# Kernel tuning notes

Hardware: AMD Instinct MI355X
Metric: run time of the kernel (lower is better)

The kernel has to match this reference:

```python
import jax, jax.numpy as jnp
import numpy as np

B, T, I, H = 64, 512, 1024, 2048


def setup_inputs() -> dict:
    key = jax.random.key(0)
    ks = jax.random.split(key, 6)
    s = 1.0 / np.sqrt(H).astype(np.float32)
    return {
        "input": jax.random.normal(ks[0], (B, T, I), jnp.float32),
        "internal": jax.random.normal(ks[1], (B, T), jnp.float32) * 0.1,
        "w_ih": jax.random.uniform(ks[2], (H, I), jnp.float32, -s, s),
        "w_hh": jax.random.uniform(ks[3], (H, H), jnp.float32, -s, s),
        "b_ih": jax.random.uniform(ks[4], (H,), jnp.float32, -s, s),
        "b_hh": jax.random.uniform(ks[5], (H,), jnp.float32, -s, s),
        "h0": jnp.zeros((1, B, H), jnp.float32),
        "trunc": 64,
    }


def reference(input, internal, w_ih, w_hh, b_ih, b_hh, h0, trunc):
    # input: [B, T, I]; internal: [B, T] scalar-per-step drive; h0: [1, B, H]
    Tlen = input.shape[1]
    # Hoist the input projection out of the recurrence (same math, one big GEMM).
    x_proj = jnp.einsum('bti,hi->bth', input, w_ih) + b_ih  # [B, T, H]
    # Truncated-BPTT boundaries: state is detached when i % trunc == 0.
    detach_mask = (jnp.arange(Tlen) % trunc) == 0  # [T] bool

    def step(h, xs):
        xp, noise, m = xs  # xp: [B, H], noise: [B], m: scalar bool
        # detach state at truncation boundary (no-op in forward pass)
        h = jnp.where(m, jax.lax.stop_gradient(h), h)
        h_new = jnp.tanh(xp + noise[:, None] + h @ w_hh.T + b_hh)
        return h_new, h_new

    h_last, outs = jax.lax.scan(
        step, h0[0], (x_proj.transpose(1, 0, 2), internal.T, detach_mask))
    # outputs: [B, T, H], final state: [1, B, H]
    return outs.transpose(1, 0, 2), h_last[None]
```

## Files before the change

kernel.cpp:

```cpp
#include <hip/hip_runtime.h>
#include <hip/hip_bf16.h>
#include <math.h>

#define Bb 64
#define Tt 512
#define Ii 1024
#define Hh 2048
#define NBLK 128

typedef __attribute__((ext_vector_type(8))) short bf16x8;
typedef __attribute__((ext_vector_type(8))) unsigned short ushort8;
typedef __attribute__((ext_vector_type(4))) float f32x4;

__device__ __forceinline__ unsigned short f2bf(float x) {
    unsigned int u = __float_as_uint(x);
    unsigned int r = u + 0x7fffu + ((u >> 16) & 1u);
    return (unsigned short)(r >> 16);
}

__global__ __launch_bounds__(256) void cvt_kernel(
    const float* __restrict__ src, unsigned short* __restrict__ dst)
{
    const int i = (blockIdx.x * 256 + threadIdx.x) * 4;
    float4 v = *(const float4*)(src + i);
    ushort4 o;
    o.x = f2bf(v.x); o.y = f2bf(v.y); o.z = f2bf(v.z); o.w = f2bf(v.w);
    *(ushort4*)(dst + i) = o;
}

__global__ __launch_bounds__(1024) void init_flags(unsigned int* flags) {
    flags[threadIdx.x] = 0u;
}

__global__ __launch_bounds__(256, 2) void xproj_kernel(
    const float* __restrict__ A,
    const unsigned short* __restrict__ Wbf,
    const float* __restrict__ bias,
    float* __restrict__ out)
{
    __shared__ unsigned short As[128 * 40];
    __shared__ unsigned short Bs[128 * 40];

    const int tid  = threadIdx.x;
    const int lane = tid & 63;
    const int wid  = tid >> 6;
    const int wm   = wid & 1;
    const int wn   = wid >> 1;
    const int rlo  = lane & 15;
    const int khi  = lane >> 4;

    const int m0 = blockIdx.y * 128;
    const int n0 = blockIdx.x * 128;

    f32x4 acc[4][4];
    #pragma unroll
    for (int i = 0; i < 4; ++i)
        #pragma unroll
        for (int j = 0; j < 4; ++j) acc[i][j] = (f32x4)0.f;

    for (int k0 = 0; k0 < Ii; k0 += 32) {
        #pragma unroll
        for (int p = 0; p < 4; ++p) {
            const int flat = p * 256 + tid;
            const int row  = flat >> 3;
            const int c4   = flat & 7;
            float4 v = *(const float4*)(A + (size_t)(m0 + row) * Ii + k0 + c4 * 4);
            ushort4 o;
            o.x = f2bf(v.x); o.y = f2bf(v.y); o.z = f2bf(v.z); o.w = f2bf(v.w);
            *(ushort4*)(As + row * 40 + c4 * 4) = o;
        }
        #pragma unroll
        for (int p = 0; p < 2; ++p) {
            const int flat = p * 256 + tid;
            const int row  = flat >> 2;
            const int c8   = flat & 3;
            ushort8 v = *(const ushort8*)(Wbf + (size_t)(n0 + row) * Ii + k0 + c8 * 8);
            *(ushort8*)(Bs + row * 40 + c8 * 8) = v;
        }
        __syncthreads();

        bf16x8 af[4], bfr[4];
        #pragma unroll
        for (int i = 0; i < 4; ++i)
            af[i] = *(const bf16x8*)(As + (wm * 64 + i * 16 + rlo) * 40 + khi * 8);
        #pragma unroll
        for (int j = 0; j < 4; ++j)
            bfr[j] = *(const bf16x8*)(Bs + (wn * 64 + j * 16 + rlo) * 40 + khi * 8);
        #pragma unroll
        for (int i = 0; i < 4; ++i)
            #pragma unroll
            for (int j = 0; j < 4; ++j)
                acc[i][j] = __builtin_amdgcn_mfma_f32_16x16x32_bf16(
                    af[i], bfr[j], acc[i][j], 0, 0, 0);
        __syncthreads();
    }

    #pragma unroll
    for (int j = 0; j < 4; ++j) {
        const int col = n0 + wn * 64 + j * 16 + rlo;
        const float bj = bias[col];
        #pragma unroll
        for (int i = 0; i < 4; ++i) {
            #pragma unroll
            for (int r = 0; r < 4; ++r) {
                const int m = m0 + wm * 64 + i * 16 + khi * 4 + r;
                out[(size_t)m * Hh + col] = acc[i][j][r] + bj;
            }
        }
    }
}

#define LD_FRAG(dst, base, OFF)                                               \
    asm volatile("global_load_dwordx4 %0, %1, off offset:" OFF " sc0 sc1"     \
                 : "=v"(dst) : "v"(base))

#define LD_FRAG_C(dst, base, OFF)                                             \
    asm volatile("global_load_dwordx4 %0, %1, off offset:" OFF                \
                 : "=v"(dst) : "v"(base))

#define DRAIN16(a)                                                            \
    asm volatile("s_waitcnt vmcnt(0)"                                         \
                 : "+v"(a[0][0]), "+v"(a[0][1]), "+v"(a[0][2]), "+v"(a[0][3]),\
                   "+v"(a[0][4]), "+v"(a[0][5]), "+v"(a[0][6]), "+v"(a[0][7]),\
                   "+v"(a[1][0]), "+v"(a[1][1]), "+v"(a[1][2]), "+v"(a[1][3]),\
                   "+v"(a[1][4]), "+v"(a[1][5]), "+v"(a[1][6]), "+v"(a[1][7]) \
                 :: "memory");                                                \
    __builtin_amdgcn_sched_barrier(0)

#define RAW_BARRIER()                                                         \
    asm volatile("s_waitcnt lgkmcnt(0)\n\ts_barrier" ::: "memory")

__global__ __launch_bounds__(512, 2) void rnn_persistent(
    const unsigned short* __restrict__ w_bf,
    unsigned short* __restrict__ h_bf,
    const float* __restrict__ b_hh,
    const float* __restrict__ internal,
    float* __restrict__ out,
    unsigned int* __restrict__ flags)
{
    __shared__ f32x4 red4[8 * 256];

    const int tid  = threadIdx.x;
    const int lane = tid & 63;
    const int wid  = tid >> 6;
    const int rlo  = lane & 15;
    const int khi  = lane >> 4;
    const int blk  = blockIdx.x;
    const int rh   = blk & 1;
    const int cg   = blk >> 1;

    bf16x8 wf[2][8];
    {
        const unsigned short* w0 =
            w_bf + (size_t)(cg * 32 + rlo) * Hh + wid * 256 + khi * 8;
        const unsigned short* w1 = w0 + (size_t)16 * Hh;
        LD_FRAG_C(wf[0][0], w0, "0");   LD_FRAG_C(wf[0][1], w0, "64");
        LD_FRAG_C(wf[0][2], w0, "128"); LD_FRAG_C(wf[0][3], w0, "192");
        LD_FRAG_C(wf[0][4], w0, "256"); LD_FRAG_C(wf[0][5], w0, "320");
        LD_FRAG_C(wf[0][6], w0, "384"); LD_FRAG_C(wf[0][7], w0, "448");
        LD_FRAG_C(wf[1][0], w1, "0");   LD_FRAG_C(wf[1][1], w1, "64");
        LD_FRAG_C(wf[1][2], w1, "128"); LD_FRAG_C(wf[1][3], w1, "192");
        LD_FRAG_C(wf[1][4], w1, "256"); LD_FRAG_C(wf[1][5], w1, "320");
        LD_FRAG_C(wf[1][6], w1, "384"); LD_FRAG_C(wf[1][7], w1, "448");
        DRAIN16(wf);
    }

    const int em    = (tid >> 6) & 1;
    const int ent   = (tid >> 7) & 1;
    const int odd   = lane & 1;
    const int clloc = (ent * 16 + rlo) & ~1;
    const int cl    = cg * 32 + clloc;
    const int rAl   = em * 16 + khi * 4 + 2 * odd;
    const int rAg   = rh * 32 + rAl;
    const int rBg   = rAg + 1;
    const float2 bh2 = (tid < 256) ? *(const float2*)(b_hh + cl)
                                   : make_float2(0.f, 0.f);

    float2 xpA = make_float2(0.f, 0.f), xpB = make_float2(0.f, 0.f);
    float  nzA = 0.f, nzB = 0.f;
    if (tid < 256) {
        xpA = *(const float2*)(out + ((size_t)rAg * Tt + 0) * Hh + cl);
        xpB = *(const float2*)(out + ((size_t)rBg * Tt + 0) * Hh + cl);
        nzA = internal[rAg * Tt + 0];
        nzB = internal[rBg * Tt + 0];
    }
    float2 gA_d = make_float2(0.f, 0.f), gB_d = make_float2(0.f, 0.f);

    unsigned int* myflag   = flags + blk * 4 + wid;
    unsigned int* aggbase  = flags + 8 * lane + 4 * rh;
    unsigned int* rootst   = flags + 512 + (rh * 16 + lane) * 16;
    unsigned int* rootpoll = flags + 512 + (rh * 16 + ((blk >> 1) & 15)) * 16;

    for (int t = 0; t < Tt; ++t) {
        const bool last = (t == Tt - 1);
        const unsigned short* h_cur = h_bf + (size_t)(t & 1) * Bb * Hh;
        unsigned short*       h_nxt = h_bf + (size_t)((t + 1) & 1) * Bb * Hh;

        const unsigned short* am0 =
            h_cur + (size_t)(rh * 32 + rlo) * Hh + wid * 256 + khi * 8;
        const unsigned short* am1 = am0 + (size_t)16 * Hh;

        bf16x8 a[2][8];
        LD_FRAG(a[0][0], am0, "0");   LD_FRAG(a[0][1], am0, "64");
        LD_FRAG(a[0][2], am0, "128"); LD_FRAG(a[0][3], am0, "192");
        LD_FRAG(a[0][4], am0, "256"); LD_FRAG(a[0][5], am0, "320");
        LD_FRAG(a[0][6], am0, "384"); LD_FRAG(a[0][7], am0, "448");
        LD_FRAG(a[1][0], am1, "0");   LD_FRAG(a[1][1], am1, "64");
        LD_FRAG(a[1][2], am1, "128"); LD_FRAG(a[1][3], am1, "192");
        LD_FRAG(a[1][4], am1, "256"); LD_FRAG(a[1][5], am1, "320");
        LD_FRAG(a[1][6], am1, "384"); LD_FRAG(a[1][7], am1, "448");

        if (tid < 256 && t > 0) {
            *(float2*)(out + ((size_t)rAg * Tt + (t - 1)) * Hh + cl) = gA_d;
            *(float2*)(out + ((size_t)rBg * Tt + (t - 1)) * Hh + cl) = gB_d;
        }

        DRAIN16(a);

        f32x4 acc[2][2];
        #pragma unroll
        for (int m = 0; m < 2; ++m)
            #pragma unroll
            for (int nt = 0; nt < 2; ++nt) acc[m][nt] = (f32x4)0.f;
        #pragma unroll
        for (int kk = 0; kk < 8; ++kk)
            #pragma unroll
            for (int m = 0; m < 2; ++m)
                #pragma unroll
                for (int nt = 0; nt < 2; ++nt)
                    acc[m][nt] = __builtin_amdgcn_mfma_f32_16x16x32_bf16(
                        a[m][kk], wf[nt][kk], acc[m][nt], 0, 0, 0);

        #pragma unroll
        for (int nt = 0; nt < 2; ++nt)
            #pragma unroll
            for (int m = 0; m < 2; ++m)
                red4[wid * 256 + (nt * 2 + m) * 64 + lane] = acc[m][nt];
        RAW_BARRIER();

        if (tid < 256) {
            f32x4 s4 = (f32x4)0.f;
            #pragma unroll
            for (int ks = 0; ks < 8; ++ks)
                s4 += red4[ks * 256 + tid];

            f32x4 o4;
            #pragma unroll
            for (int i = 0; i < 4; ++i)
                o4[i] = __shfl_xor(s4[i], 1, 64);

            const float sA_lo = odd ? o4[2] : s4[0];
            const float sA_hi = odd ? s4[2] : o4[0];
            const float sB_lo = odd ? o4[3] : s4[1];
            const float sB_hi = odd ? s4[3] : o4[1];

            float2 gA, gB;
            gA.x = tanhf(xpA.x + nzA + bh2.x + sA_lo);
            gA.y = tanhf(xpA.y + nzA + bh2.y + sA_hi);
            gB.x = tanhf(xpB.x + nzB + bh2.x + sB_lo);
            gB.y = tanhf(xpB.y + nzB + bh2.y + sB_hi);

            const unsigned int hpA =
                (unsigned int)f2bf(gA.x) | ((unsigned int)f2bf(gA.y) << 16);
            const unsigned int hpB =
                (unsigned int)f2bf(gB.x) | ((unsigned int)f2bf(gB.y) << 16);
            __hip_atomic_store((unsigned int*)h_nxt + ((size_t)rAg * Hh + cl) / 2,
                               hpA, __ATOMIC_RELAXED, __HIP_MEMORY_SCOPE_AGENT);
            __hip_atomic_store((unsigned int*)h_nxt + ((size_t)rBg * Hh + cl) / 2,
                               hpB, __ATOMIC_RELAXED, __HIP_MEMORY_SCOPE_AGENT);

            if (last) {
                *(float2*)(out + ((size_t)rAg * Tt + t) * Hh + cl) = gA;
                *(float2*)(out + ((size_t)rBg * Tt + t) * Hh + cl) = gB;
                float* tail = out + (size_t)Bb * Tt * Hh;
                *(float2*)(tail + (size_t)rAg * Hh + cl) = gA;
                *(float2*)(tail + (size_t)rBg * Hh + cl) = gB;
            } else {
                gA_d = gA; gB_d = gB;

                asm volatile("s_waitcnt vmcnt(0)" ::: "memory");
                if (lane == 0)
                    __hip_atomic_store(myflag, (unsigned int)(t + 1),
                                       __ATOMIC_RELAXED,
                                       __HIP_MEMORY_SCOPE_AGENT);

                xpA = *(const float2*)(out + ((size_t)rAg * Tt + t + 1) * Hh + cl);
                xpB = *(const float2*)(out + ((size_t)rBg * Tt + t + 1) * Hh + cl);
                nzA = internal[rAg * Tt + t + 1];
                nzB = internal[rBg * Tt + t + 1];
            }
        }
        if (last) break;

        const unsigned int tgt = (unsigned int)(t + 1);
        if (blk < 2 && wid == 7) {
            unsigned int f0, f1, f2, f3;
            while (true) {
                asm volatile("global_load_dword %0, %1, off sc0 sc1"
                             : "=v"(f0) : "v"(aggbase));
                asm volatile("global_load_dword %0, %1, off offset:4 sc0 sc1"
                             : "=v"(f1) : "v"(aggbase));
                asm volatile("global_load_dword %0, %1, off offset:8 sc0 sc1"
                             : "=v"(f2) : "v"(aggbase));
                asm volatile("global_load_dword %0, %1, off offset:12 sc0 sc1"
                             : "=v"(f3) : "v"(aggbase));
                asm volatile("s_waitcnt vmcnt(0)"
                             : "+v"(f0), "+v"(f1), "+v"(f2), "+v"(f3)
                             :: "memory");
                if (__all(f0 >= tgt && f1 >= tgt && f2 >= tgt && f3 >= tgt))
                    break;
                __builtin_amdgcn_s_sleep(1);
            }
            if (lane < 16)
                __hip_atomic_store(rootst, tgt, __ATOMIC_RELAXED,
                                   __HIP_MEMORY_SCOPE_AGENT);
        } else if (wid == 7) {
            while (__hip_atomic_load(rootpoll, __ATOMIC_RELAXED,
                                     __HIP_MEMORY_SCOPE_AGENT) < tgt)
                __builtin_amdgcn_s_sleep(1);
        }
        RAW_BARRIER();
    }
}

extern "C" void kernel_launch(void* const* d_in, const int* in_sizes, int n_in,
                              void* d_out, int out_size, void* d_ws, size_t ws_size,
                              hipStream_t stream) {
    const float* input    = (const float*)d_in[0];
    const float* internal = (const float*)d_in[1];
    const float* w_ih     = (const float*)d_in[2];
    const float* w_hh     = (const float*)d_in[3];
    const float* b_ih     = (const float*)d_in[4];
    const float* b_hh     = (const float*)d_in[5];
    const float* h0       = (const float*)d_in[6];
    float* out = (float*)d_out;

    unsigned short* w_hh_bf = (unsigned short*)d_ws;
    unsigned short* w_ih_bf = w_hh_bf + (size_t)Hh * Hh;
    unsigned short* h_bf    = w_ih_bf + (size_t)Hh * Ii;
    unsigned int*   flags   = (unsigned int*)(h_bf + (size_t)2 * Bb * Hh);

    hipLaunchKernelGGL(init_flags, dim3(1), dim3(1024), 0, stream, flags);
    hipLaunchKernelGGL(cvt_kernel, dim3((Hh * Hh) / 1024), dim3(256), 0, stream,
                       w_hh, w_hh_bf);
    hipLaunchKernelGGL(cvt_kernel, dim3((Hh * Ii) / 1024), dim3(256), 0, stream,
                       w_ih, w_ih_bf);
    hipLaunchKernelGGL(cvt_kernel, dim3((Bb * Hh) / 1024), dim3(256), 0, stream,
                       h0, h_bf);

    dim3 g1(Hh / 128, (Bb * Tt) / 128);
    hipLaunchKernelGGL(xproj_kernel, g1, dim3(256), 0, stream,
                       input, w_ih_bf, b_ih, out);

    void* args[] = {(void*)&w_hh_bf, (void*)&h_bf, (void*)&b_hh,
                    (void*)&internal, (void*)&out, (void*)&flags};
    hipLaunchCooperativeKernel((void*)rnn_persistent, dim3(NBLK), dim3(512),
                               args, 0, stream);
}
```

Before: 3.809 ms.

## Fuse input projection into persistent RNN kernel with register-resident W_ih slice

Removes the separate x-projection GEMM and instead has each persistent block keep its W_ih slice in registers and compute the x·W_ih contribution for the next timestep inside the recurrence loop, overlapping it with the sync wait. Input is first converted to bf16 into workspace, and both biases are folded together. This avoids writing and re-reading the fp32 x_proj through the output buffer, but adds per-step input loads and MFMA work to the latency-critical loop, plus register pressure. The old path is kept as a fallback when the workspace is too small.

```diff
diff --git a/kernel.cpp b/kernel.cpp
--- a/kernel.cpp
+++ b/kernel.cpp
@@ -21,7 +21,7 @@
 __global__ __launch_bounds__(256) void cvt_kernel(
     const float* __restrict__ src, unsigned short* __restrict__ dst)
 {
-    const int i = (blockIdx.x * 256 + threadIdx.x) * 4;
+    const size_t i = ((size_t)blockIdx.x * 256 + threadIdx.x) * 4;
     float4 v = *(const float4*)(src + i);
     ushort4 o;
     o.x = f2bf(v.x); o.y = f2bf(v.y); o.z = f2bf(v.z); o.w = f2bf(v.w);
@@ -127,12 +127,22 @@
                  :: "memory");                                                \
     __builtin_amdgcn_sched_barrier(0)
 
+#define DRAIN8(x)                                                             \
+    asm volatile("s_waitcnt vmcnt(0)"                                         \
+                 : "+v"(x[0][0]), "+v"(x[0][1]), "+v"(x[0][2]), "+v"(x[0][3]),\
+                   "+v"(x[1][0]), "+v"(x[1][1]), "+v"(x[1][2]), "+v"(x[1][3]) \
+                 :: "memory");                                                \
+    __builtin_amdgcn_sched_barrier(0)
+
 #define RAW_BARRIER()                                                         \
     asm volatile("s_waitcnt lgkmcnt(0)\n\ts_barrier" ::: "memory")
 
-__global__ __launch_bounds__(512, 2) void rnn_persistent(
+__global__ __launch_bounds__(512, 2) void rnn_persistent_fused(
     const unsigned short* __restrict__ w_bf,
+    const unsigned short* __restrict__ wx_bf,
+    const unsigned short* __restrict__ x_bf,
     unsigned short* __restrict__ h_bf,
+    const float* __restrict__ b_ih,
     const float* __restrict__ b_hh,
     const float* __restrict__ internal,
     float* __restrict__ out,
@@ -164,6 +174,17 @@
         LD_FRAG_C(wf[1][6], w1, "384"); LD_FRAG_C(wf[1][7], w1, "448");
         DRAIN16(wf);
     }
+    bf16x8 wxr[2][4];
+    {
+        const unsigned short* q0 =
+            wx_bf + (size_t)(cg * 32 + rlo) * Ii + wid * 128 + khi * 8;
+        const unsigned short* q1 = q0 + (size_t)16 * Ii;
+        LD_FRAG_C(wxr[0][0], q0, "0");   LD_FRAG_C(wxr[0][1], q0, "64");
+        LD_FRAG_C(wxr[0][2], q0, "128"); LD_FRAG_C(wxr[0][3], q0, "192");
+        LD_FRAG_C(wxr[1][0], q1, "0");   LD_FRAG_C(wxr[1][1], q1, "64");
+        LD_FRAG_C(wxr[1][2], q1, "128"); LD_FRAG_C(wxr[1][3], q1, "192");
+        DRAIN8(wxr);
+    }
 
     const int em    = (tid >> 6) & 1;
     const int ent   = (tid >> 7) & 1;
@@ -173,14 +194,12 @@
     const int rAl   = em * 16 + khi * 4 + 2 * odd;
     const int rAg   = rh * 32 + rAl;
     const int rBg   = rAg + 1;
-    const float2 bh2 = (tid < 256) ? *(const float2*)(b_hh + cl)
-                                   : make_float2(0.f, 0.f);
-
-    float2 xpA = make_float2(0.f, 0.f), xpB = make_float2(0.f, 0.f);
+    float2 bh2 = make_float2(0.f, 0.f);
     float  nzA = 0.f, nzB = 0.f;
     if (tid < 256) {
-        xpA = *(const float2*)(out + ((size_t)rAg * Tt + 0) * Hh + cl);
-        xpB = *(const float2*)(out + ((size_t)rBg * Tt + 0) * Hh + cl);
+        const float2 bi = *(const float2*)(b_ih + cl);
+        const float2 bh = *(const float2*)(b_hh + cl);
+        bh2 = make_float2(bi.x + bh.x, bi.y + bh.y);
         nzA = internal[rAg * Tt + 0];
         nzB = internal[rBg * Tt + 0];
     }
@@ -190,6 +209,33 @@
     unsigned int* aggbase  = flags + 8 * lane + 4 * rh;
     unsigned int* rootst   = flags + 512 + (rh * 16 + lane) * 16;
     unsigned int* rootpoll = flags + 512 + (rh * 16 + ((blk >> 1) & 15)) * 16;
+
+    const unsigned short* xm0 =
+        x_bf + (size_t)(rh * 32 + rlo) * (Tt * Ii) + wid * 128 + khi * 8;
+    const unsigned short* xm1 = xm0 + (size_t)16 * (Tt * Ii);
+
+    f32x4 acc_x[2][2];
+    {
+        bf16x8 xa[2][4];
+        LD_FRAG_C(xa[0][0], xm0, "0");   LD_FRAG_C(xa[0][1], xm0, "64");
+        LD_FRAG_C(xa[0][2], xm0, "128"); LD_FRAG_C(xa[0][3], xm0, "192");
+        LD_FRAG_C(xa[1][0], xm1, "0");   LD_FRAG_C(xa[1][1], xm1, "64");
+        LD_FRAG_C(xa[1][2], xm1, "128"); LD_FRAG_C(xa[1][3], xm1, "192");
+        DRAIN8(xa);
+        #pragma unroll
+        for (int m = 0; m < 2; ++m)
+            #pragma unroll
+            for (int nt = 0; nt < 2; ++nt) acc_x[m][nt] = (f32x4)0.f;
+        #pragma unroll
+        for (int kk = 0; kk < 4; ++kk)
+            #pragma unroll
+            for (int m = 0; m < 2; ++m)
+                #pragma unroll
+                for (int nt = 0; nt < 2; ++nt)
+                    acc_x[m][nt] = __builtin_amdgcn_mfma_f32_16x16x32_bf16(
+                        xa[m][kk], wxr[nt][kk], acc_x[m][nt], 0, 0, 0);
+        xm0 += Ii; xm1 += Ii;
+    }
 
     for (int t = 0; t < Tt; ++t) {
         const bool last = (t == Tt - 1);
@@ -210,18 +256,28 @@
         LD_FRAG(a[1][4], am1, "256"); LD_FRAG(a[1][5], am1, "320");
         LD_FRAG(a[1][6], am1, "384"); LD_FRAG(a[1][7], am1, "448");
 
+        bf16x8 xa[2][4];
+        if (!last) {
+            LD_FRAG_C(xa[0][0], xm0, "0");   LD_FRAG_C(xa[0][1], xm0, "64");
+            LD_FRAG_C(xa[0][2], xm0, "128"); LD_FRAG_C(xa[0][3], xm0, "192");
+            LD_FRAG_C(xa[1][0], xm1, "0");   LD_FRAG_C(xa[1][1], xm1, "64");
+            LD_FRAG_C(xa[1][2], xm1, "128"); LD_FRAG_C(xa[1][3], xm1, "192");
+            xm0 += Ii; xm1 += Ii;
+        }
+
         if (tid < 256 && t > 0) {
             *(float2*)(out + ((size_t)rAg * Tt + (t - 1)) * Hh + cl) = gA_d;
             *(float2*)(out + ((size_t)rBg * Tt + (t - 1)) * Hh + cl) = gB_d;
         }
 
         DRAIN16(a);
+        if (!last) { DRAIN8(xa); }
 
         f32x4 acc[2][2];
         #pragma unroll
         for (int m = 0; m < 2; ++m)
             #pragma unroll
-            for (int nt = 0; nt < 2; ++nt) acc[m][nt] = (f32x4)0.f;
+            for (int nt = 0; nt < 2; ++nt) acc[m][nt] = acc_x[m][nt];
         #pragma unroll
         for (int kk = 0; kk < 8; ++kk)
             #pragma unroll
@@ -255,10 +311,10 @@
             const float sB_hi = odd ? s4[3] : o4[1];
 
             float2 gA, gB;
-            gA.x = tanhf(xpA.x + nzA + bh2.x + sA_lo);
-            gA.y = tanhf(xpA.y + nzA + bh2.y + sA_hi);
-            gB.x = tanhf(xpB.x + nzB + bh2.x + sB_lo);
-            gB.y = tanhf(xpB.y + nzB + bh2.y + sB_hi);
+            gA.x = tanhf(nzA + bh2.x + sA_lo);
+            gA.y = tanhf(nzA + bh2.y + sA_hi);
+            gB.x = tanhf(nzB + bh2.x + sB_lo);
+            gB.y = tanhf(nzB + bh2.y + sB_hi);
 
             const unsigned int hpA =
                 (unsigned int)f2bf(gA.x) | ((unsigned int)f2bf(gA.y) << 16);
@@ -277,18 +333,29 @@
                 *(float2*)(tail + (size_t)rBg * Hh + cl) = gB;
             } else {
                 gA_d = gA; gB_d = gB;
-
                 asm volatile("s_waitcnt vmcnt(0)" ::: "memory");
                 if (lane == 0)
                     __hip_atomic_store(myflag, (unsigned int)(t + 1),
                                        __ATOMIC_RELAXED,
                                        __HIP_MEMORY_SCOPE_AGENT);
-
-                xpA = *(const float2*)(out + ((size_t)rAg * Tt + t + 1) * Hh + cl);
-                xpB = *(const float2*)(out + ((size_t)rBg * Tt + t + 1) * Hh + cl);
                 nzA = internal[rAg * Tt + t + 1];
                 nzB = internal[rBg * Tt + t + 1];
             }
+        }
+
+        if (!last) {
+            #pragma unroll
+            for (int m = 0; m < 2; ++m)
+                #pragma unroll
+                for (int nt = 0; nt < 2; ++nt) acc_x[m][nt] = (f32x4)0.f;
+            #pragma unroll
+            for (int kk = 0; kk < 4; ++kk)
+                #pragma unroll
+                for (int m = 0; m < 2; ++m)
+                    #pragma unroll
+                    for (int nt = 0; nt < 2; ++nt)
+                        acc_x[m][nt] = __builtin_amdgcn_mfma_f32_16x16x32_bf16(
+                            xa[m][kk], wxr[nt][kk], acc_x[m][nt], 0, 0, 0);
         }
         if (last) break;
 
@@ -323,6 +390,197 @@
     }
 }
 
+__global__ __launch_bounds__(512, 2) void rnn_persistent_fb(
+    const unsigned short* __restrict__ w_bf,
+    unsigned short* __restrict__ h_bf,
+    const float* __restrict__ b_hh,
+    const float* __restrict__ internal,
+    float* __restrict__ out,
+    unsigned int* __restrict__ flags)
+{
+    __shared__ f32x4 red4[8 * 256];
+
+    const int tid  = threadIdx.x;
+    const int lane = tid & 63;
+    const int wid  = tid >> 6;
+    const int rlo  = lane & 15;
+    const int khi  = lane >> 4;
+    const int blk  = blockIdx.x;
+    const int rh   = blk & 1;
+    const int cg   = blk >> 1;
+
+    bf16x8 wf[2][8];
+    {
+        const unsigned short* w0 =
+            w_bf + (size_t)(cg * 32 + rlo) * Hh + wid * 256 + khi * 8;
+        const unsigned short* w1 = w0 + (size_t)16 * Hh;
+        LD_FRAG_C(wf[0][0], w0, "0");   LD_FRAG_C(wf[0][1], w0, "64");
+        LD_FRAG_C(wf[0][2], w0, "128"); LD_FRAG_C(wf[0][3], w0, "192");
+        LD_FRAG_C(wf[0][4], w0, "256"); LD_FRAG_C(wf[0][5], w0, "320");
+        LD_FRAG_C(wf[0][6], w0, "384"); LD_FRAG_C(wf[0][7], w0, "448");
+        LD_FRAG_C(wf[1][0], w1, "0");   LD_FRAG_C(wf[1][1], w1, "64");
+        LD_FRAG_C(wf[1][2], w1, "128"); LD_FRAG_C(wf[1][3], w1, "192");
+        LD_FRAG_C(wf[1][4], w1, "256"); LD_FRAG_C(wf[1][5], w1, "320");
+        LD_FRAG_C(wf[1][6], w1, "384"); LD_FRAG_C(wf[1][7], w1, "448");
+        DRAIN16(wf);
+    }
+
+    const int em    = (tid >> 6) & 1;
+    const int ent   = (tid >> 7) & 1;
+    const int odd   = lane & 1;
+    const int clloc = (ent * 16 + rlo) & ~1;
+    const int cl    = cg * 32 + clloc;
+    const int rAl   = em * 16 + khi * 4 + 2 * odd;
+    const int rAg   = rh * 32 + rAl;
+    const int rBg   = rAg + 1;
+    const float2 bh2 = (tid < 256) ? *(const float2*)(b_hh + cl)
+                                   : make_float2(0.f, 0.f);
+
+    float2 xpA = make_float2(0.f, 0.f), xpB = make_float2(0.f, 0.f);
+    float  nzA = 0.f, nzB = 0.f;
+    if (tid < 256) {
+        xpA = *(const float2*)(out + ((size_t)rAg * Tt + 0) * Hh + cl);
+        xpB = *(const float2*)(out + ((size_t)rBg * Tt + 0) * Hh + cl);
+        nzA = internal[rAg * Tt + 0];
+        nzB = internal[rBg * Tt + 0];
+    }
+    float2 gA_d = make_float2(0.f, 0.f), gB_d = make_float2(0.f, 0.f);
+
+    unsigned int* myflag   = flags + blk * 4 + wid;
+    unsigned int* aggbase  = flags + 8 * lane + 4 * rh;
+    unsigned int* rootst   = flags + 512 + (rh * 16 + lane) * 16;
+    unsigned int* rootpoll = flags + 512 + (rh * 16 + ((blk >> 1) & 15)) * 16;
+
+    for (int t = 0; t < Tt; ++t) {
+        const bool last = (t == Tt - 1);
+        const unsigned short* h_cur = h_bf + (size_t)(t & 1) * Bb * Hh;
+        unsigned short*       h_nxt = h_bf + (size_t)((t + 1) & 1) * Bb * Hh;
+
+        const unsigned short* am0 =
+            h_cur + (size_t)(rh * 32 + rlo) * Hh + wid * 256 + khi * 8;
+        const unsigned short* am1 = am0 + (size_t)16 * Hh;
+
+        bf16x8 a[2][8];
+        LD_FRAG(a[0][0], am0, "0");   LD_FRAG(a[0][1], am0, "64");
+        LD_FRAG(a[0][2], am0, "128"); LD_FRAG(a[0][3], am0, "192");
+        LD_FRAG(a[0][4], am0, "256"); LD_FRAG(a[0][5], am0, "320");
+        LD_FRAG(a[0][6], am0, "384"); LD_FRAG(a[0][7], am0, "448");
+        LD_FRAG(a[1][0], am1, "0");   LD_FRAG(a[1][1], am1, "64");
+        LD_FRAG(a[1][2], am1, "128"); LD_FRAG(a[1][3], am1, "192");
+        LD_FRAG(a[1][4], am1, "256"); LD_FRAG(a[1][5], am1, "320");
+        LD_FRAG(a[1][6], am1, "384"); LD_FRAG(a[1][7], am1, "448");
+
+        if (tid < 256 && t > 0) {
+            *(float2*)(out + ((size_t)rAg * Tt + (t - 1)) * Hh + cl) = gA_d;
+            *(float2*)(out + ((size_t)rBg * Tt + (t - 1)) * Hh + cl) = gB_d;
+        }
+
+        DRAIN16(a);
+
+        f32x4 acc[2][2];
+        #pragma unroll
+        for (int m = 0; m < 2; ++m)
+            #pragma unroll
+            for (int nt = 0; nt < 2; ++nt) acc[m][nt] = (f32x4)0.f;
+        #pragma unroll
+        for (int kk = 0; kk < 8; ++kk)
+            #pragma unroll
+            for (int m = 0; m < 2; ++m)
+                #pragma unroll
+                for (int nt = 0; nt < 2; ++nt)
+                    acc[m][nt] = __builtin_amdgcn_mfma_f32_16x16x32_bf16(
+                        a[m][kk], wf[nt][kk], acc[m][nt], 0, 0, 0);
+
+        #pragma unroll
+        for (int nt = 0; nt < 2; ++nt)
+            #pragma unroll
+            for (int m = 0; m < 2; ++m)
+                red4[wid * 256 + (nt * 2 + m) * 64 + lane] = acc[m][nt];
+        RAW_BARRIER();
+
+        if (tid < 256) {
+            f32x4 s4 = (f32x4)0.f;
+            #pragma unroll
+            for (int ks = 0; ks < 8; ++ks)
+                s4 += red4[ks * 256 + tid];
+
+            f32x4 o4;
+            #pragma unroll
+            for (int i = 0; i < 4; ++i)
+                o4[i] = __shfl_xor(s4[i], 1, 64);
+
+            const float sA_lo = odd ? o4[2] : s4[0];
+            const float sA_hi = odd ? s4[2] : o4[0];
+            const float sB_lo = odd ? o4[3] : s4[1];
+            const float sB_hi = odd ? s4[3] : o4[1];
+
+            float2 gA, gB;
+            gA.x = tanhf(xpA.x + nzA + bh2.x + sA_lo);
+            gA.y = tanhf(xpA.y + nzA + bh2.y + sA_hi);
+            gB.x = tanhf(xpB.x + nzB + bh2.x + sB_lo);
+            gB.y = tanhf(xpB.y + nzB + bh2.y + sB_hi);
+
+            const unsigned int hpA =
+                (unsigned int)f2bf(gA.x) | ((unsigned int)f2bf(gA.y) << 16);
+            const unsigned int hpB =
+                (unsigned int)f2bf(gB.x) | ((unsigned int)f2bf(gB.y) << 16);
+            __hip_atomic_store((unsigned int*)h_nxt + ((size_t)rAg * Hh + cl) / 2,
+                               hpA, __ATOMIC_RELAXED, __HIP_MEMORY_SCOPE_AGENT);
+            __hip_atomic_store((unsigned int*)h_nxt + ((size_t)rBg * Hh + cl) / 2,
+                               hpB, __ATOMIC_RELAXED, __HIP_MEMORY_SCOPE_AGENT);
+
+            if (last) {
+                *(float2*)(out + ((size_t)rAg * Tt + t) * Hh + cl) = gA;
+                *(float2*)(out + ((size_t)rBg * Tt + t) * Hh + cl) = gB;
+                float* tail = out + (size_t)Bb * Tt * Hh;
+                *(float2*)(tail + (size_t)rAg * Hh + cl) = gA;
+                *(float2*)(tail + (size_t)rBg * Hh + cl) = gB;
+            } else {
+                gA_d = gA; gB_d = gB;
+                asm volatile("s_waitcnt vmcnt(0)" ::: "memory");
+                if (lane == 0)
+                    __hip_atomic_store(myflag, (unsigned int)(t + 1),
+                                       __ATOMIC_RELAXED,
+                                       __HIP_MEMORY_SCOPE_AGENT);
+                xpA = *(const float2*)(out + ((size_t)rAg * Tt + t + 1) * Hh + cl);
+                xpB = *(const float2*)(out + ((size_t)rBg * Tt + t + 1) * Hh + cl);
+                nzA = internal[rAg * Tt + t + 1];
+                nzB = internal[rBg * Tt + t + 1];
+            }
+        }
+        if (last) break;
+
+        const unsigned int tgt = (unsigned int)(t + 1);
+        if (blk < 2 && wid == 7) {
+            unsigned int f0, f1, f2, f3;
+            while (true) {
+                asm volatile("global_load_dword %0, %1, off sc0 sc1"
+                             : "=v"(f0) : "v"(aggbase));
+                asm volatile("global_load_dword %0, %1, off offset:4 sc0 sc1"
+                             : "=v"(f1) : "v"(aggbase));
+                asm volatile("global_load_dword %0, %1, off offset:8 sc0 sc1"
+                             : "=v"(f2) : "v"(aggbase));
+                asm volatile("global_load_dword %0, %1, off offset:12 sc0 sc1"
+                             : "=v"(f3) : "v"(aggbase));
+                asm volatile("s_waitcnt vmcnt(0)"
+                             : "+v"(f0), "+v"(f1), "+v"(f2), "+v"(f3)
+                             :: "memory");
+                if (__all(f0 >= tgt && f1 >= tgt && f2 >= tgt && f3 >= tgt))
+                    break;
+                __builtin_amdgcn_s_sleep(1);
+            }
+            if (lane < 16)
+                __hip_atomic_store(rootst, tgt, __ATOMIC_RELAXED,
+                                   __HIP_MEMORY_SCOPE_AGENT);
+        } else if (wid == 7) {
+            while (__hip_atomic_load(rootpoll, __ATOMIC_RELAXED,
+                                     __HIP_MEMORY_SCOPE_AGENT) < tgt)
+                __builtin_amdgcn_s_sleep(1);
+        }
+        RAW_BARRIER();
+    }
+}
+
 extern "C" void kernel_launch(void* const* d_in, const int* in_sizes, int n_in,
                               void* d_out, int out_size, void* d_ws, size_t ws_size,
                               hipStream_t stream) {
@@ -335,25 +593,53 @@
     const float* h0       = (const float*)d_in[6];
     float* out = (float*)d_out;
 
+    const size_t usW  = (size_t)Hh * Hh;
+    const size_t usWx = (size_t)Hh * Ii;
+    const size_t usH  = (size_t)2 * Bb * Hh;
+    const size_t usX  = (size_t)Bb * Tt * Ii;
+    const size_t need_fused = (usW + usWx + usH + usX) * 2 + 1024 * 4 + 256;
+
     unsigned short* w_hh_bf = (unsigned short*)d_ws;
-    unsigned short* w_ih_bf = w_hh_bf + (size_t)Hh * Hh;
-    unsigned short* h_bf    = w_ih_bf + (size_t)Hh * Ii;
-    unsigned int*   flags   = (unsigned int*)(h_bf + (size_t)2 * Bb * Hh);
-
-    hipLaunchKernelGGL(init_flags, dim3(1), dim3(1024), 0, stream, flags);
-    hipLaunchKernelGGL(cvt_kernel, dim3((Hh * Hh) / 1024), dim3(256), 0, stream,
-                       w_hh, w_hh_bf);
-    hipLaunchKernelGGL(cvt_kernel, dim3((Hh * Ii) / 1024), dim3(256), 0, stream,
-                       w_ih, w_ih_bf);
-    hipLaunchKernelGGL(cvt_kernel, dim3((Bb * Hh) / 1024), dim3(256), 0, stream,
-                       h0, h_bf);
-
-    dim3 g1(Hh / 128, (Bb * Tt) / 128);
-    hipLaunchKernelGGL(xproj_kernel, g1, dim3(256), 0, stream,
-                       input, w_ih_bf, b_ih, out);
-
-    void* args[] = {(void*)&w_hh_bf, (void*)&h_bf, (void*)&b_hh,
-                    (void*)&internal, (void*)&out, (void*)&flags};
-    hipLaunchCooperativeKernel((void*)rnn_persistent, dim3(NBLK), dim3(512),
-                               args, 0, stream);
+    unsigned short* w_ih_bf = w_hh_bf + usW;
+    unsigned short* h_bf    = w_ih_bf + usWx;
+
+    if (ws_size >= need_fused) {
+        unsigned short* x_bf  = h_bf + usH;
+        unsigned int*   flags = (unsigned int*)(x_bf + usX);
+
+        hipLaunchKernelGGL(init_flags, dim3(1), dim3(1024), 0, stream, flags);
+        hipLaunchKernelGGL(cvt_kernel, dim3((Hh * Hh) / 1024), dim3(256), 0,
+                           stream, w_hh, w_hh_bf);
+        hipLaunchKernelGGL(cvt_kernel, dim3((Hh * Ii) / 1024), dim3(256), 0,
+                           stream, w_ih, w_ih_bf);
+        hipLaunchKernelGGL(cvt_kernel, dim3((Bb * Hh) / 1024), dim3(256), 0,
+                           stream, h0, h_bf);
+        hipLaunchKernelGGL(cvt_kernel, dim3((Bb * Tt * Ii) / 1024), dim3(256), 0,
+                           stream, input, x_bf);
+
+        void* args[] = {(void*)&w_hh_bf, (void*)&w_ih_bf, (void*)&x_bf,
+                        (void*)&h_bf, (void*)&b_ih, (void*)&b_hh,
+                        (void*)&internal, (void*)&out, (void*)&flags};
+        hipLaunchCooperativeKernel((void*)rnn_persistent_fused, dim3(NBLK),
+                                   dim3(512), args, 0, stream);
+    } else {
+        unsigned int* flags = (unsigned int*)(h_bf + usH);
+
+        hipLaunchKernelGGL(init_flags, dim3(1), dim3(1024), 0, stream, flags);
+        hipLaunchKernelGGL(cvt_kernel, dim3((Hh * Hh) / 1024), dim3(256), 0,
+                           stream, w_hh, w_hh_bf);
+        hipLaunchKernelGGL(cvt_kernel, dim3((Hh * Ii) / 1024), dim3(256), 0,
+                           stream, w_ih, w_ih_bf);
+        hipLaunchKernelGGL(cvt_kernel, dim3((Bb * Hh) / 1024), dim3(256), 0,
+                           stream, h0, h_bf);
+
+        dim3 g1(Hh / 128, (Bb * Tt) / 128);
+        hipLaunchKernelGGL(xproj_kernel, g1, dim3(256), 0, stream,
+                           input, w_ih_bf, b_ih, out);
+
+        void* args[] = {(void*)&w_hh_bf, (void*)&h_bf, (void*)&b_hh,
+                        (void*)&internal, (void*)&out, (void*)&flags};
+        hipLaunchCooperativeKernel((void*)rnn_persistent_fb, dim3(NBLK),
+                                   dim3(512), args, 0, stream);
+    }
 }
```

Result: slower. 4.556 ms (+19.6%).
